# Performance work log

Measured on AMD Instinct MI355X. Metric: run time of the kernel, lower is better.

The kernel has to match this reference:

```python
import jax, jax.numpy as jnp
import numpy as np

B, S, IN, D, H, L, M = 8, 1024, 256, 512, 8, 2, 64
DK = D // H
FF = 4 * D
EPS = 1e-5


def setup_inputs() -> dict:
    key = jax.random.key(0)
    ks = jax.random.split(key, 16)
    w = lambda k, shape: jax.random.normal(k, shape, jnp.float32) * 0.02
    return {
        "inputs": jax.random.normal(ks[0], (B, S, IN), jnp.float32),
        "lengths": jax.random.randint(ks[1], (B,), S // 2, S + 1),
        "W_in": w(ks[2], (IN, D)), "b_in": jnp.zeros((D,), jnp.float32),
        # per-layer stacked params (leading axis L) for lax.scan
        "Wq": w(ks[3], (L, D, D)), "bq": jnp.zeros((L, D), jnp.float32),
        "Wk": w(ks[4], (L, D, D)), "bk": jnp.zeros((L, D), jnp.float32),
        "Wv": w(ks[5], (L, D, D)), "bv": jnp.zeros((L, D), jnp.float32),
        "Wo": w(ks[6], (L, D, D)), "bo": jnp.zeros((L, D), jnp.float32),
        "rel_bias": w(ks[7], (L, H, 2 * M - 1)),
        "W1": w(ks[8], (L, D, FF)), "b1": jnp.zeros((L, FF), jnp.float32),
        "W2": w(ks[9], (L, FF, D)), "b2": jnp.zeros((L, D), jnp.float32),
        "g1": jnp.ones((L, D), jnp.float32), "be1": jnp.zeros((L, D), jnp.float32),
        "g2": jnp.ones((L, D), jnp.float32), "be2": jnp.zeros((L, D), jnp.float32),
        "gf": jnp.ones((D,), jnp.float32), "bef": jnp.zeros((D,), jnp.float32),
    }


def _ln(x, g, b):
    m = jnp.mean(x, axis=-1, keepdims=True)
    v = jnp.mean(jnp.square(x - m), axis=-1, keepdims=True)
    return (x - m) * jax.lax.rsqrt(v + EPS) * g + b


def _sinusoid_pe(seq_len, d_model):
    pos = jnp.arange(seq_len, dtype=jnp.float32)[:, None]
    div = jnp.exp(jnp.arange(0, d_model, 2, dtype=jnp.float32) * (-np.log(10000.0) / d_model))
    pe = jnp.zeros((seq_len, d_model), jnp.float32)
    pe = pe.at[:, 0::2].set(jnp.sin(pos * div))
    pe = pe.at[:, 1::2].set(jnp.cos(pos * div))
    return pe


def _encoder(inputs, lengths, W_in, b_in, Wq, bq, Wk, bk, Wv, bv, Wo, bo,
             rel_bias, W1, b1, W2, b2, g1, be1, g2, be2, gf, bef):
    x = inputs @ W_in + b_in                      # (B,S,D)
    x = x + _sinusoid_pe(S, D)[None]
    pad = jnp.arange(S)[None, :] >= lengths[:, None]   # (B,S) True = padded key

    r = jnp.arange(S)
    rel_idx = jnp.clip(r[:, None] - r[None, :], -(M - 1), M - 1) + (M - 1)  # (S,S)
    scale = 1.0 / np.sqrt(DK)

    def layer(x, p):
        (wq, bq_, wk, bk_, wv, bv_, wo, bo_, rb, w1, b1_, w2, b2_, g1_, be1_, g2_, be2_) = p
        # --- self-attention sublayer (pre-norm) ---
        h = _ln(x, g1_, be1_)
        q = (h @ wq + bq_).reshape(B, S, H, DK).transpose(0, 2, 1, 3)  # (B,H,S,DK)
        k = (h @ wk + bk_).reshape(B, S, H, DK).transpose(0, 2, 1, 3)
        v = (h @ wv + bv_).reshape(B, S, H, DK).transpose(0, 2, 1, 3)
        scores = jnp.einsum('bhqd,bhkd->bhqk', q, k) * scale
        scores = scores + rb[:, rel_idx][None]            # (H,S,S) relative bias
        scores = jnp.where(pad[:, None, None, :], -jnp.inf, scores)
        attn = jax.nn.softmax(scores, axis=-1)
        o = jnp.einsum('bhqk,bhkd->bhqd', attn, v)
        o = o.transpose(0, 2, 1, 3).reshape(B, S, D) @ wo + bo_
        x = x + o
        # --- FFN sublayer (pre-norm) ---
        h = _ln(x, g2_, be2_)
        x = x + (jax.nn.relu(h @ w1 + b1_) @ w2 + b2_)
        return x, None

    stacked = (Wq, bq, Wk, bk, Wv, bv, Wo, bo, rel_bias, W1, b1, W2, b2, g1, be1, g2, be2)
    x, _ = jax.lax.scan(layer, x, stacked)
    return _ln(x, gf, bef)


def reference(inputs, lengths, W_in, b_in, Wq, bq, Wk, bk, Wv, bv, Wo, bo,
              rel_bias, W1, b1, W2, b2, g1, be1, g2, be2, gf, bef):
    return _encoder(inputs, lengths, W_in, b_in, Wq, bq, Wk, bk, Wv, bv, Wo, bo,
                    rel_bias, W1, b1, W2, b2, g1, be1, g2, be2, gf, bef)
```

## Files before the change

### kernel.cpp

```cpp
#include <hip/hip_runtime.h>
#include <hip/hip_bf16.h>

typedef unsigned short u16;
typedef unsigned int u32;
typedef __bf16 v8bf __attribute__((ext_vector_type(8)));
typedef float v4f __attribute__((ext_vector_type(4)));

#define B_SZ 8
#define S_LEN 1024
#define IN_DIM 256
#define DMODEL 512
#define NHEAD 8
#define DK 64
#define FF_DIM 2048
#define MROWS (B_SZ * S_LEN)
#define QSCALE 0.1803368801111204f

__device__ __forceinline__ u16 f2bf(float f) {
    unsigned int x = __float_as_uint(f);
    unsigned int r = (x + 0x7fffu + ((x >> 16) & 1u)) >> 16;
    return (u16)r;
}

__device__ __forceinline__ void gl16(const u16* g, u16* l) {
    __builtin_amdgcn_global_load_lds((const __attribute__((address_space(1))) unsigned int*)g,
                                     (__attribute__((address_space(3))) unsigned int*)l, 16, 0, 0);
}

__global__ __launch_bounds__(256) void conv_bf16_kernel(const float* __restrict__ in,
                                                        u16* __restrict__ out, int n4) {
    int i = blockIdx.x * 256 + threadIdx.x;
    if (i < n4) {
        float4 v = ((const float4*)in)[i];
        ushort4 o;
        o.x = f2bf(v.x); o.y = f2bf(v.y); o.z = f2bf(v.z); o.w = f2bf(v.w);
        ((ushort4*)out)[i] = o;
    }
}

struct TDesc { const float* src; u16* dst; int K; int N; };
struct TArgs { TDesc d[13]; };

__global__ void transpose_conv_kernel(TArgs args) {
    TDesc t = args.d[blockIdx.z];
    int k0 = blockIdx.x * 32, n0 = blockIdx.y * 32;
    if (k0 >= t.K || n0 >= t.N) return;
    __shared__ float tile[32][33];
    int tx = threadIdx.x, ty = threadIdx.y;
#pragma unroll
    for (int j = 0; j < 4; j++) {
        int k = k0 + ty + j * 8;
        tile[ty + j * 8][tx] = t.src[(size_t)k * t.N + n0 + tx];
    }
    __syncthreads();
#pragma unroll
    for (int j = 0; j < 4; j++) {
        int n = n0 + ty + j * 8;
        t.dst[(size_t)n * t.K + k0 + tx] = f2bf(tile[tx][ty + j * 8]);
    }
}

template <bool OUT_BF16>
__global__ __launch_bounds__(256) void ln_kernel(const float* __restrict__ x,
                                                 const float* __restrict__ g,
                                                 const float* __restrict__ b,
                                                 void* __restrict__ out) {
    int row = blockIdx.x * 4 + (threadIdx.x >> 6);
    int lane = threadIdx.x & 63;
    const float4* xr = (const float4*)(x + (size_t)row * DMODEL);
    float4 v0 = xr[lane], v1 = xr[lane + 64];
    float s = v0.x + v0.y + v0.z + v0.w + v1.x + v1.y + v1.z + v1.w;
    float sq = v0.x * v0.x + v0.y * v0.y + v0.z * v0.z + v0.w * v0.w +
               v1.x * v1.x + v1.y * v1.y + v1.z * v1.z + v1.w * v1.w;
#pragma unroll
    for (int m = 1; m < 64; m <<= 1) {
        s += __shfl_xor(s, m);
        sq += __shfl_xor(sq, m);
    }
    float mean = s * (1.0f / DMODEL);
    float var = sq * (1.0f / DMODEL) - mean * mean;
    float rstd = rsqrtf(var + 1e-5f);
    const float4* g4 = (const float4*)g;
    const float4* b4 = (const float4*)b;
    float4 ga = g4[lane], gb = g4[lane + 64], ba = b4[lane], bb = b4[lane + 64];
    float4 r0, r1;
    r0.x = (v0.x - mean) * rstd * ga.x + ba.x;
    r0.y = (v0.y - mean) * rstd * ga.y + ba.y;
    r0.z = (v0.z - mean) * rstd * ga.z + ba.z;
    r0.w = (v0.w - mean) * rstd * ga.w + ba.w;
    r1.x = (v1.x - mean) * rstd * gb.x + bb.x;
    r1.y = (v1.y - mean) * rstd * gb.y + bb.y;
    r1.z = (v1.z - mean) * rstd * gb.z + bb.z;
    r1.w = (v1.w - mean) * rstd * gb.w + bb.w;
    if (OUT_BF16) {
        ushort4 o0, o1;
        o0.x = f2bf(r0.x); o0.y = f2bf(r0.y); o0.z = f2bf(r0.z); o0.w = f2bf(r0.w);
        o1.x = f2bf(r1.x); o1.y = f2bf(r1.y); o1.z = f2bf(r1.z); o1.w = f2bf(r1.w);
        ((ushort4*)out)[(size_t)row * 128 + lane] = o0;
        ((ushort4*)out)[(size_t)row * 128 + 64 + lane] = o1;
    } else {
        ((float4*)out)[(size_t)row * 128 + lane] = r0;
        ((float4*)out)[(size_t)row * 128 + 64 + lane] = r1;
    }
}

template <int MT, int NT>
__device__ __forceinline__ void gemm_core(const u16* __restrict__ A, const u16* __restrict__ Bt,
                                          int K, v4f (&acc)[MT][NT]) {
    constexpr int BM = MT * 32;
    constexpr int BN = NT * 32;
    __shared__ u16 As[BM * 64];
    __shared__ u16 Bs[BN * 64];
    int tid = threadIdx.x;
    int n0 = blockIdx.x * BN, m0 = blockIdx.y * BM;
    int w = tid >> 6, lane = tid & 63;
    int wr = (w >> 1) * (BM / 2), wc = (w & 1) * (BN / 2);
    int lr = lane & 15, lq = lane >> 4;
    int r8 = lane >> 3, cb = lane & 7;
    int scol = (cb ^ r8) * 8;

    v4f zero = {0.f, 0.f, 0.f, 0.f};
#pragma unroll
    for (int i = 0; i < MT; i++)
#pragma unroll
        for (int j = 0; j < NT; j++) acc[i][j] = zero;

    const u16* gA[MT]; u16* lA[MT];
#pragma unroll
    for (int j = 0; j < MT; j++) {
        int row0 = (MT * 8) * w + j * 8;
        gA[j] = A + (size_t)(m0 + row0 + r8) * K + scol;
        lA[j] = As + row0 * 64;
    }
    const u16* gB[NT]; u16* lB[NT];
#pragma unroll
    for (int j = 0; j < NT; j++) {
        int row0 = (NT * 8) * w + j * 8;
        gB[j] = Bt + (size_t)(n0 + row0 + r8) * K + scol;
        lB[j] = Bs + row0 * 64;
    }

    for (int k0 = 0; k0 < K; k0 += 64) {
#pragma unroll
        for (int j = 0; j < MT; j++) gl16(gA[j], lA[j]);
#pragma unroll
        for (int j = 0; j < NT; j++) gl16(gB[j], lB[j]);
        __syncthreads();
#pragma unroll
        for (int kk = 0; kk < 2; kk++) {
            int xb = ((kk * 4 + lq) ^ (lr & 7)) * 8;
            v8bf af[MT], bfr[NT];
#pragma unroll
            for (int i = 0; i < MT; i++)
                af[i] = *(const v8bf*)&As[(wr + i * 16 + lr) * 64 + xb];
#pragma unroll
            for (int j = 0; j < NT; j++)
                bfr[j] = *(const v8bf*)&Bs[(wc + j * 16 + lr) * 64 + xb];
#pragma unroll
            for (int mt = 0; mt < MT; mt++)
#pragma unroll
                for (int nt = 0; nt < NT; nt++)
                    acc[mt][nt] = __builtin_amdgcn_mfma_f32_16x16x32_bf16(af[mt], bfr[nt], acc[mt][nt], 0, 0, 0);
        }
        __syncthreads();
#pragma unroll
        for (int j = 0; j < MT; j++) gA[j] += 64;
#pragma unroll
        for (int j = 0; j < NT; j++) gB[j] += 64;
    }
}

__global__ __launch_bounds__(256) void gemm_in_kernel(const u16* __restrict__ A,
                                                      const u16* __restrict__ Bt,
                                                      const float* __restrict__ bias,
                                                      float* __restrict__ Out, int K) {
    v4f acc[4][2];
    gemm_core<4, 2>(A, Bt, K, acc);
    int tid = threadIdx.x, w = tid >> 6, lane = tid & 63;
    int lr = lane & 15, lq = lane >> 4;
    int wr = (w >> 1) * 64, wc = (w & 1) * 32;
    int n0 = blockIdx.x * 64, m0 = blockIdx.y * 128;
#pragma unroll
    for (int mt = 0; mt < 4; mt++) {
#pragma unroll
        for (int nt = 0; nt < 2; nt++) {
            int col = n0 + wc + nt * 16 + lr;
            float bcol = bias[col];
            float freq = __builtin_amdgcn_exp2f((float)(col & ~1) * (-0.025953277f));
#pragma unroll
            for (int reg = 0; reg < 4; reg++) {
                int row = m0 + wr + mt * 16 + lq * 4 + reg;
                float rev = (float)(row & (S_LEN - 1)) * freq * 0.15915494309189535f;
                float fr = __builtin_amdgcn_fractf(rev);
                float pe = (col & 1) ? __builtin_amdgcn_cosf(fr) : __builtin_amdgcn_sinf(fr);
                Out[(size_t)row * DMODEL + col] = acc[mt][nt][reg] + bcol + pe;
            }
        }
    }
}

__global__ __launch_bounds__(256) void gemm_qkv_kernel(const u16* __restrict__ A,
                                                       const u16* __restrict__ Bt,
                                                       const float* __restrict__ bq,
                                                       const float* __restrict__ bk,
                                                       const float* __restrict__ bv,
                                                       u16* __restrict__ Qo,
                                                       u16* __restrict__ Ko,
                                                       u16* __restrict__ Vto, int K) {
    v4f acc[4][4];
    gemm_core<4, 4>(A, Bt, K, acc);
    int tid = threadIdx.x, w = tid >> 6, lane = tid & 63;
    int lr = lane & 15, lq = lane >> 4;
    int wr = (w >> 1) * 64, wc = (w & 1) * 64;
    int n0 = blockIdx.x * 128, m0 = blockIdx.y * 128;
    int seg = n0 >> 9;
#pragma unroll
    for (int mt = 0; mt < 4; mt++) {
#pragma unroll
        for (int nt = 0; nt < 4; nt++) {
            int col = (n0 + wc + nt * 16 + lr) & (DMODEL - 1);
            if (seg == 0) {
                float bcol = bq[col];
#pragma unroll
                for (int reg = 0; reg < 4; reg++) {
                    int row = m0 + wr + mt * 16 + lq * 4 + reg;
                    Qo[(size_t)row * DMODEL + col] = f2bf((acc[mt][nt][reg] + bcol) * QSCALE);
                }
            } else if (seg == 1) {
                float bcol = bk[col];
#pragma unroll
                for (int reg = 0; reg < 4; reg++) {
                    int row = m0 + wr + mt * 16 + lq * 4 + reg;
                    Ko[(size_t)row * DMODEL + col] = f2bf(acc[mt][nt][reg] + bcol);
                }
            } else {
                float bcol = bv[col];
                int row0 = m0 + wr + mt * 16 + lq * 4;
                int bb = row0 >> 10, s0 = row0 & (S_LEN - 1);
                ushort4 o;
                o.x = f2bf(acc[mt][nt][0] + bcol);
                o.y = f2bf(acc[mt][nt][1] + bcol);
                o.z = f2bf(acc[mt][nt][2] + bcol);
                o.w = f2bf(acc[mt][nt][3] + bcol);
                *(ushort4*)(Vto + ((size_t)(bb * DMODEL + col)) * S_LEN + s0) = o;
            }
        }
    }
}

__global__ __launch_bounds__(256) void gemm_relu_kernel(const u16* __restrict__ A,
                                                        const u16* __restrict__ Bt,
                                                        const float* __restrict__ bias,
                                                        u16* __restrict__ Out, int N, int K) {
    v4f acc[4][4];
    gemm_core<4, 4>(A, Bt, K, acc);
    int tid = threadIdx.x, w = tid >> 6, lane = tid & 63;
    int lr = lane & 15, lq = lane >> 4;
    int wr = (w >> 1) * 64, wc = (w & 1) * 64;
    int n0 = blockIdx.x * 128, m0 = blockIdx.y * 128;
#pragma unroll
    for (int mt = 0; mt < 4; mt++) {
#pragma unroll
        for (int nt = 0; nt < 4; nt++) {
            int col = n0 + wc + nt * 16 + lr;
            float bcol = bias[col];
#pragma unroll
            for (int reg = 0; reg < 4; reg++) {
                int row = m0 + wr + mt * 16 + lq * 4 + reg;
                Out[(size_t)row * N + col] = f2bf(fmaxf(acc[mt][nt][reg] + bcol, 0.0f));
            }
        }
    }
}

__global__ __launch_bounds__(256) void gemm_res_kernel(const u16* __restrict__ A,
                                                       const u16* __restrict__ Bt,
                                                       const float* __restrict__ bias,
                                                       float* __restrict__ Out, int K) {
    v4f acc[4][2];
    gemm_core<4, 2>(A, Bt, K, acc);
    int tid = threadIdx.x, w = tid >> 6, lane = tid & 63;
    int lr = lane & 15, lq = lane >> 4;
    int wr = (w >> 1) * 64, wc = (w & 1) * 32;
    int n0 = blockIdx.x * 64, m0 = blockIdx.y * 128;
#pragma unroll
    for (int mt = 0; mt < 4; mt++) {
#pragma unroll
        for (int nt = 0; nt < 2; nt++) {
            int col = n0 + wc + nt * 16 + lr;
            float bcol = bias[col];
#pragma unroll
            for (int reg = 0; reg < 4; reg++) {
                int row = m0 + wr + mt * 16 + lq * 4 + reg;
                size_t idx = (size_t)row * DMODEL + col;
                Out[idx] = Out[idx] + acc[mt][nt][reg] + bcol;
            }
        }
    }
}

#define LDP 68
__global__ __launch_bounds__(256) void fattn_kernel(const u16* __restrict__ Qg,
                                                    const u16* __restrict__ Kg,
                                                    const u16* __restrict__ Vtg,
                                                    const float* __restrict__ rb,
                                                    const int* __restrict__ lengths,
                                                    u16* __restrict__ O) {
    int qt = blockIdx.x, h = blockIdx.y, b = blockIdx.z;
    int tid = threadIdx.x, w = tid >> 6, lane = tid & 63;
    int lr = lane & 15, lq = lane >> 4;
    __shared__ u16 Ks[2][64 * 64];
    __shared__ u16 Vs[2][64 * 64];
    __shared__ u16 Pw[4][32 * LDP];
    __shared__ float rbs[128];
    int len = lengths[b];
    if (tid < 127) rbs[tid] = rb[h * 127 + tid] * 1.4426950408889634f;

    int qw = qt * 128 + w * 32;
    v8bf qa[2][2];
#pragma unroll
    for (int ntq = 0; ntq < 2; ntq++) {
        size_t qrow = ((size_t)(b * S_LEN + qw + ntq * 16 + lr)) * DMODEL + h * DK;
        qa[ntq][0] = *(const v8bf*)(Qg + qrow + lq * 8);
        qa[ntq][1] = *(const v8bf*)(Qg + qrow + 32 + lq * 8);
    }

    v4f zero = {0.f, 0.f, 0.f, 0.f};
    v4f Oacc[2][4];
#pragma unroll
    for (int mt = 0; mt < 2; mt++)
#pragma unroll
        for (int nt = 0; nt < 4; nt++) Oacc[mt][nt] = zero;
    float lsum[2] = {0.f, 0.f};

    const u16* Kbase = Kg + ((size_t)b * S_LEN) * DMODEL + h * DK;
    const u16* Vbase = Vtg + ((size_t)(b * DMODEL + h * DK)) * S_LEN;
    u16* P = Pw[w];
    int r8 = lane >> 3, cb = lane & 7;
    int swz = (cb ^ r8) * 8;

#pragma unroll
    for (int j = 0; j < 2; j++) {
        int row0 = w * 16 + j * 8;
        gl16(Kbase + (size_t)(row0 + r8) * DMODEL + swz, Ks[0] + row0 * 64);
        gl16(Vbase + (size_t)(row0 + r8) * S_LEN + swz, Vs[0] + row0 * 64);
    }

    int pb = 0;
    for (int kb0 = 0; kb0 < len; kb0 += 64, pb ^= 1) {
        __syncthreads();

        int nxt = kb0 + 64;
        if (nxt < len) {
#pragma unroll
            for (int j = 0; j < 2; j++) {
                int row0 = w * 16 + j * 8;
                gl16(Kbase + (size_t)(nxt + row0 + r8) * DMODEL + swz, Ks[pb ^ 1] + row0 * 64);
                gl16(Vbase + (size_t)(row0 + r8) * S_LEN + nxt + swz, Vs[pb ^ 1] + row0 * 64);
            }
        }
        const u16* Ksc = Ks[pb];
        const u16* Vsc = Vs[pb];

        v8bf kf[4][2];
#pragma unroll
        for (int mtk = 0; mtk < 4; mtk++) {
#pragma unroll
            for (int half = 0; half < 2; half++) {
                int xb = ((half * 4 + lq) ^ (lr & 7)) * 8;
                kf[mtk][half] = *(const v8bf*)&Ksc[(mtk * 16 + lr) * 64 + xb];
            }
        }

        v4f S[4][2];
#pragma unroll
        for (int mtk = 0; mtk < 4; mtk++)
#pragma unroll
            for (int ntq = 0; ntq < 2; ntq++) {
                v4f s = __builtin_amdgcn_mfma_f32_16x16x32_bf16(kf[mtk][0], qa[ntq][0], zero, 0, 0, 0);
                S[mtk][ntq] = __builtin_amdgcn_mfma_f32_16x16x32_bf16(kf[mtk][1], qa[ntq][1], s, 0, 0, 0);
            }

        bool edge = (kb0 + 64 > len);
        int dmin = qw - (kb0 + 63), dmax = qw + 31 - kb0;
        bool perel = !(dmax <= -63 || dmin >= 63);
        float bconst = (dmax <= -63) ? rbs[0] : rbs[126];
#pragma unroll
        for (int mtk = 0; mtk < 4; mtk++) {
#pragma unroll
            for (int ntq = 0; ntq < 2; ntq++) {
                int q = qw + ntq * 16 + lr;
                float p[4];
#pragma unroll
                for (int r = 0; r < 4; r++) {
                    int key = kb0 + mtk * 16 + lq * 4 + r;
                    float s = S[mtk][ntq][r];
                    if (perel) {
                        int d = q - key;
                        d = d < -63 ? -63 : (d > 63 ? 63 : d);
                        s += rbs[d + 63];
                    } else {
                        s += bconst;
                    }
                    float pv = __builtin_amdgcn_exp2f(s);
                    if (edge && key >= len) pv = 0.f;
                    lsum[ntq] += pv;
                    p[r] = pv;
                }
                uint2 pk;
                pk.x = (__float_as_uint(p[1]) & 0xffff0000u) | (__float_as_uint(p[0]) >> 16);
                pk.y = (__float_as_uint(p[3]) & 0xffff0000u) | (__float_as_uint(p[2]) >> 16);
                *(uint2*)&P[(ntq * 16 + lr) * LDP + mtk * 16 + lq * 4] = pk;
            }
        }

        v8bf vb[4][2];
#pragma unroll
        for (int ntd = 0; ntd < 4; ntd++) {
#pragma unroll
            for (int half = 0; half < 2; half++) {
                int xb = ((half * 4 + lq) ^ (lr & 7)) * 8;
                vb[ntd][half] = *(const v8bf*)&Vsc[(ntd * 16 + lr) * 64 + xb];
            }
        }
#pragma unroll
        for (int mtq = 0; mtq < 2; mtq++) {
            v8bf pa0 = *(const v8bf*)&P[(mtq * 16 + lr) * LDP + lq * 8];
            v8bf pa1 = *(const v8bf*)&P[(mtq * 16 + lr) * LDP + 32 + lq * 8];
#pragma unroll
            for (int ntd = 0; ntd < 4; ntd++) {
                Oacc[mtq][ntd] = __builtin_amdgcn_mfma_f32_16x16x32_bf16(pa0, vb[ntd][0], Oacc[mtq][ntd], 0, 0, 0);
                Oacc[mtq][ntd] = __builtin_amdgcn_mfma_f32_16x16x32_bf16(pa1, vb[ntd][1], Oacc[mtq][ntd], 0, 0, 0);
            }
        }
    }

    float lsumR[2];
#pragma unroll
    for (int ntq = 0; ntq < 2; ntq++) {
        float s = lsum[ntq];
        s += __shfl_xor(s, 16);
        s += __shfl_xor(s, 32);
        lsumR[ntq] = s;
    }
#pragma unroll
    for (int mtq = 0; mtq < 2; mtq++) {
        float inv[4];
#pragma unroll
        for (int r = 0; r < 4; r++)
            inv[r] = 1.0f / __shfl(lsumR[mtq], lq * 4 + r);
        size_t obase = ((size_t)(b * S_LEN + qw + mtq * 16)) * DMODEL + h * DK;
#pragma unroll
        for (int ntd = 0; ntd < 4; ntd++)
#pragma unroll
            for (int r = 0; r < 4; r++)
                O[obase + (size_t)(lq * 4 + r) * DMODEL + ntd * 16 + lr] = f2bf(Oacc[mtq][ntd][r] * inv[r]);
    }
}

extern "C" void kernel_launch(void* const* d_in, const int* in_sizes, int n_in,
                              void* d_out, int out_size, void* d_ws, size_t ws_size,
                              hipStream_t stream) {
    const float* inputs   = (const float*)d_in[0];
    const int*   lengths  = (const int*)d_in[1];
    const float* W_in     = (const float*)d_in[2];
    const float* b_in     = (const float*)d_in[3];
    const float* Wq       = (const float*)d_in[4];
    const float* bq       = (const float*)d_in[5];
    const float* Wk       = (const float*)d_in[6];
    const float* bk       = (const float*)d_in[7];
    const float* Wv       = (const float*)d_in[8];
    const float* bv       = (const float*)d_in[9];
    const float* Wo       = (const float*)d_in[10];
    const float* bo       = (const float*)d_in[11];
    const float* rel_bias = (const float*)d_in[12];
    const float* W1       = (const float*)d_in[13];
    const float* b1       = (const float*)d_in[14];
    const float* W2       = (const float*)d_in[15];
    const float* b2       = (const float*)d_in[16];
    const float* g1       = (const float*)d_in[17];
    const float* be1      = (const float*)d_in[18];
    const float* g2       = (const float*)d_in[19];
    const float* be2      = (const float*)d_in[20];
    const float* gf       = (const float*)d_in[21];
    const float* bef      = (const float*)d_in[22];

    char* ws = (char*)d_ws;
    float* xbuf = (float*)ws;          ws += (size_t)MROWS * DMODEL * 4;
    u16* hbuf   = (u16*)ws;            ws += (size_t)MROWS * DMODEL * 2;
    u16* aobuf  = (u16*)ws;            ws += (size_t)MROWS * DMODEL * 2;
    u16* qbf    = (u16*)ws;
    u16* kbf    = qbf + (size_t)MROWS * DMODEL;
    u16* vtbf   = kbf + (size_t)MROWS * DMODEL;
    u16* tbuf   = qbf;                 ws += (size_t)MROWS * DMODEL * 4 * 3;
    u16* inbf   = (u16*)ws;            ws += (size_t)MROWS * IN_DIM * 2;
    u16* wt_in  = (u16*)ws;            ws += (size_t)DMODEL * IN_DIM * 2;
    u16 *qkvw[2], *wto[2], *wt1[2], *wt2[2];
    for (int l = 0; l < 2; l++) { qkvw[l] = (u16*)ws; ws += (size_t)3 * DMODEL * DMODEL * 2; }
    for (int l = 0; l < 2; l++) { wto[l] = (u16*)ws; ws += (size_t)DMODEL * DMODEL * 2; }
    for (int l = 0; l < 2; l++) { wt1[l] = (u16*)ws; ws += (size_t)FF_DIM * DMODEL * 2; }
    for (int l = 0; l < 2; l++) { wt2[l] = (u16*)ws; ws += (size_t)DMODEL * FF_DIM * 2; }

    TArgs ta;
    int ti = 0;
    ta.d[ti++] = {W_in, wt_in, IN_DIM, DMODEL};
    for (int l = 0; l < 2; l++) {
        ta.d[ti++] = {Wq + (size_t)l * DMODEL * DMODEL, qkvw[l], DMODEL, DMODEL};
        ta.d[ti++] = {Wk + (size_t)l * DMODEL * DMODEL, qkvw[l] + (size_t)DMODEL * DMODEL, DMODEL, DMODEL};
        ta.d[ti++] = {Wv + (size_t)l * DMODEL * DMODEL, qkvw[l] + (size_t)2 * DMODEL * DMODEL, DMODEL, DMODEL};
        ta.d[ti++] = {Wo + (size_t)l * DMODEL * DMODEL, wto[l], DMODEL, DMODEL};
        ta.d[ti++] = {W1 + (size_t)l * DMODEL * FF_DIM, wt1[l], DMODEL, FF_DIM};
        ta.d[ti++] = {W2 + (size_t)l * FF_DIM * DMODEL, wt2[l], FF_DIM, DMODEL};
    }

    conv_bf16_kernel<<<dim3((MROWS * IN_DIM / 4 + 255) / 256), 256, 0, stream>>>(
        inputs, inbf, MROWS * IN_DIM / 4);
    transpose_conv_kernel<<<dim3(64, 64, 13), dim3(32, 8), 0, stream>>>(ta);

    gemm_in_kernel<<<dim3(DMODEL / 64, MROWS / 128), 256, 0, stream>>>(
        inbf, wt_in, b_in, xbuf, IN_DIM);

    for (int l = 0; l < 2; l++) {
        ln_kernel<true><<<MROWS / 4, 256, 0, stream>>>(xbuf, g1 + l * DMODEL, be1 + l * DMODEL, hbuf);
        gemm_qkv_kernel<<<dim3(3 * DMODEL / 128, MROWS / 128), 256, 0, stream>>>(
            hbuf, qkvw[l], bq + l * DMODEL, bk + l * DMODEL, bv + l * DMODEL,
            qbf, kbf, vtbf, DMODEL);
        fattn_kernel<<<dim3(S_LEN / 128, NHEAD, B_SZ), 256, 0, stream>>>(
            qbf, kbf, vtbf, rel_bias + (size_t)l * NHEAD * 127, lengths, aobuf);
        gemm_res_kernel<<<dim3(DMODEL / 64, MROWS / 128), 256, 0, stream>>>(
            aobuf, wto[l], bo + l * DMODEL, xbuf, DMODEL);
        ln_kernel<true><<<MROWS / 4, 256, 0, stream>>>(xbuf, g2 + l * DMODEL, be2 + l * DMODEL, hbuf);
        gemm_relu_kernel<<<dim3(FF_DIM / 128, MROWS / 128), 256, 0, stream>>>(
            hbuf, wt1[l], b1 + l * FF_DIM, tbuf, FF_DIM, DMODEL);
        gemm_res_kernel<<<dim3(DMODEL / 64, MROWS / 128), 256, 0, stream>>>(
            tbuf, wt2[l], b2 + l * DMODEL, xbuf, FF_DIM);
    }
    ln_kernel<false><<<MROWS / 4, 256, 0, stream>>>(xbuf, gf, bef, d_out);
}
```

Baseline: 465.4 us.

## Split attention query tile across eight waves with sixteen rows each

```diff
diff --git a/kernel.cpp b/kernel.cpp
--- a/kernel.cpp
+++ b/kernel.cpp
@@ -300,7 +300,7 @@
 }
 
 #define LDP 68
-__global__ __launch_bounds__(256) void fattn_kernel(const u16* __restrict__ Qg,
+__global__ __launch_bounds__(512) void fattn_kernel(const u16* __restrict__ Qg,
                                                     const u16* __restrict__ Kg,
                                                     const u16* __restrict__ Vtg,
                                                     const float* __restrict__ rb,
@@ -311,40 +311,34 @@
     int lr = lane & 15, lq = lane >> 4;
     __shared__ u16 Ks[2][64 * 64];
     __shared__ u16 Vs[2][64 * 64];
-    __shared__ u16 Pw[4][32 * LDP];
+    __shared__ u16 Pw[8][16 * LDP];
     __shared__ float rbs[128];
     int len = lengths[b];
     if (tid < 127) rbs[tid] = rb[h * 127 + tid] * 1.4426950408889634f;
 
-    int qw = qt * 128 + w * 32;
-    v8bf qa[2][2];
-#pragma unroll
-    for (int ntq = 0; ntq < 2; ntq++) {
-        size_t qrow = ((size_t)(b * S_LEN + qw + ntq * 16 + lr)) * DMODEL + h * DK;
-        qa[ntq][0] = *(const v8bf*)(Qg + qrow + lq * 8);
-        qa[ntq][1] = *(const v8bf*)(Qg + qrow + 32 + lq * 8);
+    int qw = qt * 128 + w * 16;
+    v8bf qa0, qa1;
+    {
+        size_t qrow = ((size_t)(b * S_LEN + qw + lr)) * DMODEL + h * DK;
+        qa0 = *(const v8bf*)(Qg + qrow + lq * 8);
+        qa1 = *(const v8bf*)(Qg + qrow + 32 + lq * 8);
     }
 
     v4f zero = {0.f, 0.f, 0.f, 0.f};
-    v4f Oacc[2][4];
-#pragma unroll
-    for (int mt = 0; mt < 2; mt++)
-#pragma unroll
-        for (int nt = 0; nt < 4; nt++) Oacc[mt][nt] = zero;
-    float lsum[2] = {0.f, 0.f};
+    v4f Oacc[4];
+#pragma unroll
+    for (int nt = 0; nt < 4; nt++) Oacc[nt] = zero;
+    float lsum = 0.f;
 
     const u16* Kbase = Kg + ((size_t)b * S_LEN) * DMODEL + h * DK;
     const u16* Vbase = Vtg + ((size_t)(b * DMODEL + h * DK)) * S_LEN;
     u16* P = Pw[w];
     int r8 = lane >> 3, cb = lane & 7;
     int swz = (cb ^ r8) * 8;
-
-#pragma unroll
-    for (int j = 0; j < 2; j++) {
-        int row0 = w * 16 + j * 8;
-        gl16(Kbase + (size_t)(row0 + r8) * DMODEL + swz, Ks[0] + row0 * 64);
-        gl16(Vbase + (size_t)(row0 + r8) * S_LEN + swz, Vs[0] + row0 * 64);
-    }
+    int srow = w * 8;
+
+    gl16(Kbase + (size_t)(srow + r8) * DMODEL + swz, Ks[0] + srow * 64);
+    gl16(Vbase + (size_t)(srow + r8) * S_LEN + swz, Vs[0] + srow * 64);
 
     int pb = 0;
     for (int kb0 = 0; kb0 < len; kb0 += 64, pb ^= 1) {
@@ -352,12 +346,8 @@
 
         int nxt = kb0 + 64;
         if (nxt < len) {
-#pragma unroll
-            for (int j = 0; j < 2; j++) {
-                int row0 = w * 16 + j * 8;
-                gl16(Kbase + (size_t)(nxt + row0 + r8) * DMODEL + swz, Ks[pb ^ 1] + row0 * 64);
-                gl16(Vbase + (size_t)(row0 + r8) * S_LEN + nxt + swz, Vs[pb ^ 1] + row0 * 64);
-            }
+            gl16(Kbase + (size_t)(nxt + srow + r8) * DMODEL + swz, Ks[pb ^ 1] + srow * 64);
+            gl16(Vbase + (size_t)(srow + r8) * S_LEN + nxt + swz, Vs[pb ^ 1] + srow * 64);
         }
         const u16* Ksc = Ks[pb];
         const u16* Vsc = Vs[pb];
@@ -372,46 +362,41 @@
             }
         }
 
-        v4f S[4][2];
-#pragma unroll
-        for (int mtk = 0; mtk < 4; mtk++)
-#pragma unroll
-            for (int ntq = 0; ntq < 2; ntq++) {
-                v4f s = __builtin_amdgcn_mfma_f32_16x16x32_bf16(kf[mtk][0], qa[ntq][0], zero, 0, 0, 0);
-                S[mtk][ntq] = __builtin_amdgcn_mfma_f32_16x16x32_bf16(kf[mtk][1], qa[ntq][1], s, 0, 0, 0);
-            }
+        v4f S[4];
+#pragma unroll
+        for (int mtk = 0; mtk < 4; mtk++) {
+            v4f s = __builtin_amdgcn_mfma_f32_16x16x32_bf16(kf[mtk][0], qa0, zero, 0, 0, 0);
+            S[mtk] = __builtin_amdgcn_mfma_f32_16x16x32_bf16(kf[mtk][1], qa1, s, 0, 0, 0);
+        }
 
         bool edge = (kb0 + 64 > len);
-        int dmin = qw - (kb0 + 63), dmax = qw + 31 - kb0;
+        int dmin = qw - (kb0 + 63), dmax = qw + 15 - kb0;
         bool perel = !(dmax <= -63 || dmin >= 63);
         float bconst = (dmax <= -63) ? rbs[0] : rbs[126];
+        int q = qw + lr;
 #pragma unroll
         for (int mtk = 0; mtk < 4; mtk++) {
-#pragma unroll
-            for (int ntq = 0; ntq < 2; ntq++) {
-                int q = qw + ntq * 16 + lr;
-                float p[4];
-#pragma unroll
-                for (int r = 0; r < 4; r++) {
-                    int key = kb0 + mtk * 16 + lq * 4 + r;
-                    float s = S[mtk][ntq][r];
-                    if (perel) {
-                        int d = q - key;
-                        d = d < -63 ? -63 : (d > 63 ? 63 : d);
-                        s += rbs[d + 63];
-                    } else {
-                        s += bconst;
-                    }
-                    float pv = __builtin_amdgcn_exp2f(s);
-                    if (edge && key >= len) pv = 0.f;
-                    lsum[ntq] += pv;
-                    p[r] = pv;
+            float p[4];
+#pragma unroll
+            for (int r = 0; r < 4; r++) {
+                int key = kb0 + mtk * 16 + lq * 4 + r;
+                float s = S[mtk][r];
+                if (perel) {
+                    int d = q - key;
+                    d = d < -63 ? -63 : (d > 63 ? 63 : d);
+                    s += rbs[d + 63];
+                } else {
+                    s += bconst;
                 }
-                uint2 pk;
-                pk.x = (__float_as_uint(p[1]) & 0xffff0000u) | (__float_as_uint(p[0]) >> 16);
-                pk.y = (__float_as_uint(p[3]) & 0xffff0000u) | (__float_as_uint(p[2]) >> 16);
-                *(uint2*)&P[(ntq * 16 + lr) * LDP + mtk * 16 + lq * 4] = pk;
-            }
+                float pv = __builtin_amdgcn_exp2f(s);
+                if (edge && key >= len) pv = 0.f;
+                lsum += pv;
+                p[r] = pv;
+            }
+            uint2 pk;
+            pk.x = (__float_as_uint(p[1]) & 0xffff0000u) | (__float_as_uint(p[0]) >> 16);
+            pk.y = (__float_as_uint(p[3]) & 0xffff0000u) | (__float_as_uint(p[2]) >> 16);
+            *(uint2*)&P[lr * LDP + mtk * 16 + lq * 4] = pk;
         }
 
         v8bf vb[4][2];
@@ -423,39 +408,28 @@
                 vb[ntd][half] = *(const v8bf*)&Vsc[(ntd * 16 + lr) * 64 + xb];
             }
         }
-#pragma unroll
-        for (int mtq = 0; mtq < 2; mtq++) {
-            v8bf pa0 = *(const v8bf*)&P[(mtq * 16 + lr) * LDP + lq * 8];
-            v8bf pa1 = *(const v8bf*)&P[(mtq * 16 + lr) * LDP + 32 + lq * 8];
-#pragma unroll
-            for (int ntd = 0; ntd < 4; ntd++) {
-                Oacc[mtq][ntd] = __builtin_amdgcn_mfma_f32_16x16x32_bf16(pa0, vb[ntd][0], Oacc[mtq][ntd], 0, 0, 0);
-                Oacc[mtq][ntd] = __builtin_amdgcn_mfma_f32_16x16x32_bf16(pa1, vb[ntd][1], Oacc[mtq][ntd], 0, 0, 0);
-            }
-        }
-    }
-
-    float lsumR[2];
-#pragma unroll
-    for (int ntq = 0; ntq < 2; ntq++) {
-        float s = lsum[ntq];
-        s += __shfl_xor(s, 16);
-        s += __shfl_xor(s, 32);
-        lsumR[ntq] = s;
-    }
-#pragma unroll
-    for (int mtq = 0; mtq < 2; mtq++) {
-        float inv[4];
+        v8bf pa0 = *(const v8bf*)&P[lr * LDP + lq * 8];
+        v8bf pa1 = *(const v8bf*)&P[lr * LDP + 32 + lq * 8];
+#pragma unroll
+        for (int ntd = 0; ntd < 4; ntd++) {
+            Oacc[ntd] = __builtin_amdgcn_mfma_f32_16x16x32_bf16(pa0, vb[ntd][0], Oacc[ntd], 0, 0, 0);
+            Oacc[ntd] = __builtin_amdgcn_mfma_f32_16x16x32_bf16(pa1, vb[ntd][1], Oacc[ntd], 0, 0, 0);
+        }
+    }
+
+    float s = lsum;
+    s += __shfl_xor(s, 16);
+    s += __shfl_xor(s, 32);
+    float inv[4];
+#pragma unroll
+    for (int r = 0; r < 4; r++)
+        inv[r] = 1.0f / __shfl(s, lq * 4 + r);
+    size_t obase = ((size_t)(b * S_LEN + qw)) * DMODEL + h * DK;
+#pragma unroll
+    for (int ntd = 0; ntd < 4; ntd++)
 #pragma unroll
         for (int r = 0; r < 4; r++)
-            inv[r] = 1.0f / __shfl(lsumR[mtq], lq * 4 + r);
-        size_t obase = ((size_t)(b * S_LEN + qw + mtq * 16)) * DMODEL + h * DK;
-#pragma unroll
-        for (int ntd = 0; ntd < 4; ntd++)
-#pragma unroll
-            for (int r = 0; r < 4; r++)
-                O[obase + (size_t)(lq * 4 + r) * DMODEL + ntd * 16 + lr] = f2bf(Oacc[mtq][ntd][r] * inv[r]);
-    }
+            O[obase + (size_t)(lq * 4 + r) * DMODEL + ntd * 16 + lr] = f2bf(Oacc[ntd][r] * inv[r]);
 }
 
 extern "C" void kernel_launch(void* const* d_in, const int* in_sizes, int n_in,
@@ -525,7 +499,7 @@
         gemm_qkv_kernel<<<dim3(3 * DMODEL / 128, MROWS / 128), 256, 0, stream>>>(
             hbuf, qkvw[l], bq + l * DMODEL, bk + l * DMODEL, bv + l * DMODEL,
             qbf, kbf, vtbf, DMODEL);
-        fattn_kernel<<<dim3(S_LEN / 128, NHEAD, B_SZ), 256, 0, stream>>>(
+        fattn_kernel<<<dim3(S_LEN / 128, NHEAD, B_SZ), 512, 0, stream>>>(
             qbf, kbf, vtbf, rel_bias + (size_t)l * NHEAD * 127, lengths, aobuf);
         gemm_res_kernel<<<dim3(DMODEL / 64, MROWS / 128), 256, 0, stream>>>(
             aobuf, wto[l], bo + l * DMODEL, xbuf, DMODEL);
```

Result: no change. 469.5 us (+0.9%).
